# Performance work log

Hardware: AMD Instinct MI355X
Metric: run time of the kernel (lower is better)

## Reference

```python
import jax, jax.numpy as jnp
import numpy as np
import math

N_HEAD = 16
ROPE_BASE = 10000.0

def _rope_cos_sin(seq_len, head_dim, dtype):
    inv_freq = 1.0 / (ROPE_BASE ** (jnp.arange(0, head_dim, 2, dtype=jnp.float32) / head_dim))
    t = jnp.arange(seq_len, dtype=jnp.float32)
    freqs = t[:, None] * inv_freq[None, :]            # [S, D/2]
    emb = jnp.concatenate([freqs, freqs], axis=-1)     # [S, D]
    # broadcast shape [1, 1, S, D] to match q/k [B, H, S, D]
    return jnp.cos(emb)[None, None].astype(dtype), jnp.sin(emb)[None, None].astype(dtype)

def _rotate_half(x):
    x1, x2 = jnp.split(x, 2, axis=-1)
    return jnp.concatenate([-x2, x1], axis=-1)

def setup_inputs() -> dict:
    key = jax.random.key(0)
    ks = jax.random.split(key, 5)
    B, S, E = 2, 2048, 1024
    x = jax.random.normal(ks[0], (B, S, E), dtype=jnp.float32)
    init = 1.0 / math.sqrt(E)
    Wq = jax.random.normal(ks[1], (E, E), dtype=jnp.float32) * init
    Wk = jax.random.normal(ks[2], (E, E), dtype=jnp.float32) * init
    Wv = jax.random.normal(ks[3], (E, E), dtype=jnp.float32) * init
    Wo = jax.random.normal(ks[4], (E, E), dtype=jnp.float32) * init
    # causal mask: True = masked (masked_fill with -inf)
    attn_mask = jnp.triu(jnp.ones((S, S), dtype=bool), k=1)
    return {"x": x, "Wq": Wq, "Wk": Wk, "Wv": Wv, "Wo": Wo, "attn_mask": attn_mask}

def reference(x, Wq, Wk, Wv, Wo, attn_mask):
    B, S, E = x.shape
    H = N_HEAD
    D = E // H
    # projections (torch Linear: y = x @ W.T), split heads -> [B, H, S, D]
    def proj(W):
        return jnp.einsum('bse,fe->bsf', x, W).reshape(B, S, H, D).transpose(0, 2, 1, 3)
    q, k, v = proj(Wq), proj(Wk), proj(Wv)
    cos, sin = _rope_cos_sin(S, D, x.dtype)
    q = q * cos + _rotate_half(q) * sin
    k = k * cos + _rotate_half(k) * sin
    scale = 1.0 / math.sqrt(D)
    scores = jnp.einsum('bhqd,bhkd->bhqk', q, k) * scale  # [B, H, S, S]
    scores = jnp.where(attn_mask[None, None], -jnp.inf, scores)
    attn = jax.nn.softmax(scores, axis=-1)
    out = jnp.einsum('bhqk,bhkd->bhqd', attn, v)           # [B, H, S, D]
    out = out.transpose(0, 2, 1, 3).reshape(B, S, E)
    return jnp.einsum('bse,fe->bsf', out, Wo)
```

## Files before the change

### kernel.cpp

```cpp
#include <hip/hip_runtime.h>
#include <hip/hip_bf16.h>

#define NB 2
#define NH 16
#define SEQ 2048
#define HD 64
#define EMB 1024

typedef unsigned short u16;
typedef unsigned int u32;
typedef __attribute__((ext_vector_type(8))) short bf16x8;
typedef __attribute__((ext_vector_type(4))) float f32x4;
typedef __attribute__((ext_vector_type(8))) unsigned short us8;
typedef __attribute__((ext_vector_type(4))) unsigned short us4;

__device__ __forceinline__ float b2f(u16 u) {
    union { unsigned int i; float f; } v; v.i = ((unsigned int)u) << 16; return v.f;
}
__device__ __forceinline__ u16 f2b(float f) {
    union { float f; unsigned int i; } v; v.f = f;
    unsigned int x = v.i;
    return (u16)((x + 0x7FFFu + ((x >> 16) & 1u)) >> 16);
}
__device__ __forceinline__ u32 pk2(float a, float b) {
    union { __hip_bfloat162 h; u32 u; } v;
    v.h = __float22bfloat162_rn(make_float2(a, b));
    return v.u;
}

__device__ __forceinline__ void gld16(const u16* g, u16* l) {
    __builtin_amdgcn_global_load_lds((const __attribute__((address_space(1))) void*)g,
                                     (__attribute__((address_space(3))) void*)l, 16, 0, 0);
}

#define BAR8P()  asm volatile("s_barrier" ::: "memory")
#define VMW8P(n) asm volatile("s_waitcnt vmcnt(" #n ")" ::: "memory")

__device__ __forceinline__ void conv8(const void* src, u16* dst, int i, int isbf16) {
    if (isbf16) {
        *reinterpret_cast<uint4*>(dst + i) =
            *reinterpret_cast<const uint4*>((const u16*)src + i);
    } else {
        const float* s = (const float*)src + i;
        float4 a = *reinterpret_cast<const float4*>(s);
        float4 b = *reinterpret_cast<const float4*>(s + 4);
        us8 v;
        v[0] = f2b(a.x); v[1] = f2b(a.y); v[2] = f2b(a.z); v[3] = f2b(a.w);
        v[4] = f2b(b.x); v[5] = f2b(b.y); v[6] = f2b(b.z); v[7] = f2b(b.w);
        *reinterpret_cast<us8*>(dst + i) = v;
    }
}

__global__ __launch_bounds__(256)
void prep_54571854463007(const void* __restrict__ x,
                         const void* __restrict__ w0, const void* __restrict__ w1,
                         const void* __restrict__ w2, const void* __restrict__ w3,
                         u16* __restrict__ xb, u16* __restrict__ dqkv,
                         u16* __restrict__ dob, int* __restrict__ flag) {
    __shared__ int cnt;
    if (threadIdx.x == 0) cnt = 0;
    __syncthreads();
    const u16 v = ((const u16*)x)[threadIdx.x];
    const int e = (v >> 7) & 0xFF;
    if (e >= 110 && e <= 135) atomicAdd(&cnt, 1);
    __syncthreads();
    const int isbf16 = (cnt >= 200) ? 1 : 0;
    const int blk = blockIdx.x;
    if (blk == 0 && threadIdx.x == 0) *flag = isbf16;
    const int NXB = (NB * SEQ * EMB) / 2048;
    if (blk < NXB) {
        conv8(x, xb, (blk * 256 + threadIdx.x) * 8, isbf16);
    } else {
        const int r = blk - NXB;
        const int seg = r >> 9;
        const int NW = EMB * EMB;
        const void* src = (seg == 0) ? w0 : (seg == 1) ? w1 : (seg == 2) ? w2 : w3;
        u16* dst = (seg < 3) ? (dqkv + (size_t)seg * NW) : dob;
        conv8(src, dst, ((r & 511) * 256 + threadIdx.x) * 8, isbf16);
    }
}

template<int MIH, int NIH>
__device__ __forceinline__ void quad8p(const bf16x8 (&aT)[4][2], const bf16x8 (&bT)[4][2],
                                       f32x4 (&acc)[8][4]) {
#pragma unroll
    for (int i = 0; i < 4; ++i)
#pragma unroll
        for (int j = 0; j < 2; ++j)
#pragma unroll
            for (int k = 0; k < 2; ++k)
                acc[MIH * 4 + i][NIH * 2 + j] = __builtin_amdgcn_mfma_f32_16x16x32_bf16(
                    aT[i][k], bT[NIH * 2 + j][k], acc[MIH * 4 + i][NIH * 2 + j], 0, 0, 0);
}

__device__ __forceinline__ void rd8p(const u16* Ls, int buf, int rbase, int quad, int fr,
                                     bf16x8 (&dst)[4][2]) {
#pragma unroll
    for (int i = 0; i < 4; ++i) {
        const int R  = rbase + i * 16 + fr;
        const int rb = buf * 16384 + R * 64;
        const int sw = R & 7;
        dst[i][0] = *reinterpret_cast<const bf16x8*>(&Ls[rb + ((quad    ) ^ sw) * 8]);
        dst[i][1] = *reinterpret_cast<const bf16x8*>(&Ls[rb + ((quad + 4) ^ sw) * 8]);
    }
}

__global__ __launch_bounds__(512, 2)
void gemm8p_54571854463007(const u16* __restrict__ A, const u16* __restrict__ Bw,
                           u16* __restrict__ C) {
    __shared__ __align__(16) u16 As[32768];
    __shared__ __align__(16) u16 Bs[32768];
    const int tid  = threadIdx.x;
    const int w    = tid >> 6, lane = tid & 63;
    const int quad = lane >> 4, fr = lane & 15;
    const int wm   = w >> 2, wn = w & 3;
    const int m0   = blockIdx.y * 256, n0 = blockIdx.x * 256;
    const int srow = tid >> 3;
    const int schk = ((tid & 7) ^ (srow & 7)) * 8;

    auto stageU = [&](const u16* G, u16* Ls, int T, int jp, int gbase) {
        const int Tm  = T & 15;
        const int buf = T & 1;
        const int j0  = jp * 2;
        gld16(G + (size_t)(gbase + j0 * 64      + srow) * 1024 + Tm * 64 + schk,
              &Ls[buf * 16384 +  j0      * 4096 + w * 512]);
        gld16(G + (size_t)(gbase + j0 * 64 + 64 + srow) * 1024 + Tm * 64 + schk,
              &Ls[buf * 16384 + (j0 + 1) * 4096 + w * 512]);
    };

    f32x4 acc[8][4];
    const f32x4 zz = {0.f, 0.f, 0.f, 0.f};
#pragma unroll
    for (int i = 0; i < 8; ++i)
#pragma unroll
        for (int j = 0; j < 4; ++j) acc[i][j] = zz;

    stageU(A, As, 0, 0, m0);
    stageU(A, As, 0, 1, m0);
    stageU(Bw, Bs, 0, 0, n0);
    stageU(Bw, Bs, 0, 1, n0);
    stageU(A, As, 1, 0, m0);
    VMW8P(2);
    BAR8P();

#pragma unroll 1
    for (int it = 0; it < 8; ++it) {
        const int ta = 2 * it, tb = ta + 1;
        bf16x8 aT[4][2], bT[4][2];
        rd8p(As, 0, wm * 128, quad, fr, aT);
        rd8p(Bs, 0, wn * 64, quad, fr, bT);
        stageU(A, As, tb, 1, m0);
        __builtin_amdgcn_s_setprio(1); quad8p<0, 0>(aT, bT, acc); __builtin_amdgcn_s_setprio(0);
        BAR8P();
        stageU(Bw, Bs, tb, 0, n0);
        __builtin_amdgcn_s_setprio(1); quad8p<0, 1>(aT, bT, acc); __builtin_amdgcn_s_setprio(0);
        BAR8P();
        rd8p(As, 0, wm * 128 + 64, quad, fr, aT);
        stageU(Bw, Bs, tb, 1, n0);
        __builtin_amdgcn_s_setprio(1); quad8p<1, 0>(aT, bT, acc); __builtin_amdgcn_s_setprio(0);
        BAR8P();
        stageU(A, As, ta + 2, 0, m0);
        __builtin_amdgcn_s_setprio(1); quad8p<1, 1>(aT, bT, acc); __builtin_amdgcn_s_setprio(0);
        VMW8P(2);
        BAR8P();
        rd8p(As, 1, wm * 128, quad, fr, aT);
        rd8p(Bs, 1, wn * 64, quad, fr, bT);
        stageU(A, As, ta + 2, 1, m0);
        __builtin_amdgcn_s_setprio(1); quad8p<0, 0>(aT, bT, acc); __builtin_amdgcn_s_setprio(0);
        BAR8P();
        stageU(Bw, Bs, ta + 2, 0, n0);
        __builtin_amdgcn_s_setprio(1); quad8p<0, 1>(aT, bT, acc); __builtin_amdgcn_s_setprio(0);
        BAR8P();
        rd8p(As, 1, wm * 128 + 64, quad, fr, aT);
        stageU(Bw, Bs, ta + 2, 1, n0);
        __builtin_amdgcn_s_setprio(1); quad8p<1, 0>(aT, bT, acc); __builtin_amdgcn_s_setprio(0);
        BAR8P();
        stageU(A, As, tb + 2, 0, m0);
        __builtin_amdgcn_s_setprio(1); quad8p<1, 1>(aT, bT, acc); __builtin_amdgcn_s_setprio(0);
        VMW8P(2);
        BAR8P();
    }

    const int t0 = n0 >> 10;
    if (t0 == 0) {
        const float SCL = 0.18033688011112042f;
#pragma unroll
        for (int mi = 0; mi < 8; ++mi)
#pragma unroll
            for (int ni = 0; ni < 4; ++ni)
#pragma unroll
                for (int r = 0; r < 4; ++r) acc[mi][ni][r] *= SCL;
    }
    if (t0 < 2) {
        const float inv0 = __powf(10000.f, -(float)fr / 32.f);
        const float inv1 = __powf(10000.f, -(float)(fr + 16) / 32.f);
#pragma unroll
        for (int mi = 0; mi < 8; ++mi)
#pragma unroll
            for (int r = 0; r < 4; ++r) {
                const int s = (m0 + wm * 128 + mi * 16 + quad * 4 + r) & (SEQ - 1);
#pragma unroll
                for (int nl = 0; nl < 2; ++nl) {
                    float sn, cs;
                    __sincosf((float)s * (nl ? inv1 : inv0), &sn, &cs);
                    const float lo = acc[mi][nl][r], hi = acc[mi][nl + 2][r];
                    acc[mi][nl][r]     = lo * cs - hi * sn;
                    acc[mi][nl + 2][r] = hi * cs + lo * sn;
                }
            }
    }
    const size_t TS = (size_t)NB * NH * SEQ * HD;
#pragma unroll
    for (int mi = 0; mi < 8; ++mi)
#pragma unroll
        for (int ni = 0; ni < 4; ++ni)
#pragma unroll
            for (int r = 0; r < 4; ++r) {
                const int m = m0 + wm * 128 + mi * 16 + quad * 4 + r;
                const int n = n0 + wn * 64 + ni * 16 + fr;
                const int t = n >> 10, idx = n & 1023;
                const int h = idx >> 6, d = idx & 63;
                const int b = m >> 11, s = m & (SEQ - 1);
                C[t * TS + ((((size_t)b * NH + h) * SEQ + s) << 6) + d] = f2b(acc[mi][ni][r]);
            }
}

template<int OUT_MODE>
__global__ __launch_bounds__(256)
void gemm_mfma_54571854463007(const u16* __restrict__ A, const u16* __restrict__ Bw,
                              void* __restrict__ C, const int* __restrict__ flagp,
                              int M, int N, int K) {
    __shared__ __align__(16) u16 As[128 * 32];
    __shared__ __align__(16) u16 Bs[128 * 32];
    const int tid  = threadIdx.x;
    const int wave = tid >> 6, lane = tid & 63;
    const int quad = lane >> 4, fr = lane & 15;
    const int wr = (wave >> 1) * 64, wc = (wave & 1) * 64;
    const int m0 = blockIdx.y * 128, n0 = blockIdx.x * 128;
    const int r0 = tid >> 2;
    const int kc = (tid & 3) * 8;
    const f32x4 zz = {0.f, 0.f, 0.f, 0.f};
    f32x4 acc[4][4];
#pragma unroll
    for (int i = 0; i < 4; ++i)
#pragma unroll
        for (int j = 0; j < 4; ++j) acc[i][j] = zz;

    for (int k0 = 0; k0 < K; k0 += 32) {
        gld16(A  + (size_t)(m0 + r0) * K + k0 + kc,      &As[wave * 512]);
        gld16(A  + (size_t)(m0 + 64 + r0) * K + k0 + kc, &As[2048 + wave * 512]);
        gld16(Bw + (size_t)(n0 + r0) * K + k0 + kc,      &Bs[wave * 512]);
        gld16(Bw + (size_t)(n0 + 64 + r0) * K + k0 + kc, &Bs[2048 + wave * 512]);
        __syncthreads();
        bf16x8 af[4], bfr[4];
#pragma unroll
        for (int mi = 0; mi < 4; ++mi)
            af[mi] = *reinterpret_cast<const bf16x8*>(&As[(wr + mi * 16 + fr) * 32 + quad * 8]);
#pragma unroll
        for (int ni = 0; ni < 4; ++ni)
            bfr[ni] = *reinterpret_cast<const bf16x8*>(&Bs[(wc + ni * 16 + fr) * 32 + quad * 8]);
#pragma unroll
        for (int mi = 0; mi < 4; ++mi)
#pragma unroll
            for (int ni = 0; ni < 4; ++ni)
                acc[mi][ni] = __builtin_amdgcn_mfma_f32_16x16x32_bf16(af[mi], bfr[ni], acc[mi][ni], 0, 0, 0);
        __syncthreads();
    }

    const int isbf16 = *flagp;
#pragma unroll
    for (int mi = 0; mi < 4; ++mi)
#pragma unroll
        for (int ni = 0; ni < 4; ++ni)
#pragma unroll
            for (int r = 0; r < 4; ++r) {
                const int m = m0 + wr + mi * 16 + quad * 4 + r;
                const int n = n0 + wc + ni * 16 + fr;
                const float v = acc[mi][ni][r];
                if (isbf16) ((u16*)C)[(size_t)m * N + n] = f2b(v);
                else        ((float*)C)[(size_t)m * N + n] = v;
            }
}

__global__ __launch_bounds__(512, 6)
void flash_54571854463007(const u16* __restrict__ Q, const u16* __restrict__ K,
                          const u16* __restrict__ V, u16* __restrict__ AO,
                          float* __restrict__ OP0, float* __restrict__ OP1,
                          float* __restrict__ LP0, float* __restrict__ LP1) {
    __shared__ __align__(16) u16 Kt[2 * 4096];
    __shared__ __align__(16) u16 Vt[2 * 4608];
    const int tid  = threadIdx.x;
    const int w    = tid >> 6, lane = tid & 63;
    const int quad = lane >> 4, fr = lane & 15;
    const int lin = blockIdx.x;
    const int xcd = lin & 7;
    const int r_  = lin >> 3;
    const int b4  = r_ & 3;
    const int ti  = r_ >> 2;
    int T, kt0, kt1;
    if (ti < 8)       { T = 8 + ti; kt0 = 0;  kt1 = 15; }
    else if (ti == 8) { T = 15;     kt0 = 16; kt1 = 31; }
    else if (ti == 9) { T = 7;      kt0 = 0;  kt1 = 15; }
    else {
        const int g = ti - 10, s = 7 - (g >> 1);
        if ((g & 1) == 0) { T = s + 7; kt0 = 16; kt1 = 2 * T + 1; }
        else              { T = s - 1; kt0 = 0;  kt1 = 2 * T + 1; }
    }
    const bool split = (T >= 8);
    const int bh = xcd * 4 + b4;
    const int h = bh & 15, b = bh >> 4;
    const size_t base = ((size_t)b * NH + h) * SEQ * HD;
    const int k2   = (tid & 31) * 2;
    const int key0 = (k2 & 3) * 16 + (k2 >> 2);
    const int d4   = ((tid >> 5) & 15) * 4;

    const int krs = lane >> 3;
    const int kch = ((lane & 7) ^ krs) * 8;
    const int swz = fr & 7;
    const int co0 = (quad ^ swz) * 8;
    const int co1 = ((quad + 4) ^ swz) * 8;

    const bf16x8 ones = {(short)0x3F80, (short)0x3F80, (short)0x3F80, (short)0x3F80,
                         (short)0x3F80, (short)0x3F80, (short)0x3F80, (short)0x3F80};

    const u16* qp = Q + base + (size_t)(T * 128 + w * 16 + fr) * HD + quad * 8;
    const bf16x8 aq0 = *reinterpret_cast<const bf16x8*>(qp);
    const bf16x8 aq1 = *reinterpret_cast<const bf16x8*>(qp + 32);

    gld16(K + base + (size_t)(kt0 * 64 + w * 8 + krs) * HD + kch, &Kt[w * 512]);
    us4 vc0, vc1, vn0, vn1;
    {
        const u16* vs = V + base + (size_t)(kt0 * 64 + key0) * HD + d4;
        vc0 = *reinterpret_cast<const us4*>(vs);
        vc1 = *reinterpret_cast<const us4*>(vs + 16 * HD);
    }

    const f32x4 zz = {0.f, 0.f, 0.f, 0.f};
    f32x4 lacc = zz;
    f32x4 oacc[4];
#pragma unroll
    for (int nt = 0; nt < 4; ++nt) oacc[nt] = zz;

    for (int kt = kt0; kt <= kt1; ++kt) {
        const int buf = (kt - kt0) & 1;
        const int vb  = buf * 4608;
        const int kb  = buf * 4096;
#pragma unroll
        for (int jj = 0; jj < 4; ++jj) {
            const u32 pk = ((u32)(u16)vc1[jj] << 16) | (u32)(u16)vc0[jj];
            *reinterpret_cast<u32*>(&Vt[vb + (d4 + jj) * 72 + k2]) = pk;
        }
        __syncthreads();
        if (kt + 1 <= kt1) {
            const int kb1 = (buf ^ 1) * 4096;
            gld16(K + base + (size_t)((kt + 1) * 64 + w * 8 + krs) * HD + kch,
                  &Kt[kb1 + w * 512]);
            const u16* vs = V + base + (size_t)((kt + 1) * 64 + key0) * HD + d4;
            vn0 = *reinterpret_cast<const us4*>(vs);
            vn1 = *reinterpret_cast<const us4*>(vs + 16 * HD);
        }
        f32x4 sa[4];
        __builtin_amdgcn_s_setprio(1);
#pragma unroll
        for (int nt = 0; nt < 4; ++nt) {
            const int rb = kb + (nt * 16 + fr) * 64;
            const bf16x8 ka0 = *reinterpret_cast<const bf16x8*>(&Kt[rb + co0]);
            const bf16x8 ka1 = *reinterpret_cast<const bf16x8*>(&Kt[rb + co1]);
            sa[nt] = __builtin_amdgcn_mfma_f32_16x16x32_bf16(ka0, aq0, zz, 0, 0, 0);
            sa[nt] = __builtin_amdgcn_mfma_f32_16x16x32_bf16(ka1, aq1, sa[nt], 0, 0, 0);
        }
        __builtin_amdgcn_s_setprio(0);
        const int dk = kt - 2 * T;
        if (dk >= 0) {
#pragma unroll
            for (int nt = 0; nt < 4; ++nt)
#pragma unroll
                for (int r = 0; r < 4; ++r)
                    if (dk * 64 + nt * 16 + quad * 4 + r > w * 16 + fr)
                        sa[nt][r] = -__builtin_inff();
        }
        u32 c01[4], c23[4];
#pragma unroll
        for (int r = 0; r < 4; ++r) {
            c01[r] = pk2(exp2f(sa[0][r]), exp2f(sa[1][r]));
            c23[r] = pk2(exp2f(sa[2][r]), exp2f(sa[3][r]));
        }
        union { u32 u[4]; bf16x8 v; } P0, P1;
        {
            auto a = __builtin_amdgcn_permlane16_swap(c01[0], c01[2], false, false);
            auto bsw = __builtin_amdgcn_permlane32_swap(a[0], a[1], false, false);
            P0.u[0] = (u32)bsw[0]; P1.u[0] = (u32)bsw[1];
        }
        {
            auto a = __builtin_amdgcn_permlane16_swap(c23[0], c23[2], false, false);
            auto bsw = __builtin_amdgcn_permlane32_swap(a[0], a[1], false, false);
            P0.u[1] = (u32)bsw[0]; P1.u[1] = (u32)bsw[1];
        }
        {
            auto a = __builtin_amdgcn_permlane16_swap(c01[1], c01[3], false, false);
            auto bsw = __builtin_amdgcn_permlane32_swap(a[0], a[1], false, false);
            P0.u[2] = (u32)bsw[0]; P1.u[2] = (u32)bsw[1];
        }
        {
            auto a = __builtin_amdgcn_permlane16_swap(c23[1], c23[3], false, false);
            auto bsw = __builtin_amdgcn_permlane32_swap(a[0], a[1], false, false);
            P0.u[3] = (u32)bsw[0]; P1.u[3] = (u32)bsw[1];
        }
        const bf16x8 pa0 = P0.v;
        const bf16x8 pa1 = P1.v;
        __builtin_amdgcn_s_setprio(1);
        lacc = __builtin_amdgcn_mfma_f32_16x16x32_bf16(pa0, ones, lacc, 0, 0, 0);
        lacc = __builtin_amdgcn_mfma_f32_16x16x32_bf16(pa1, ones, lacc, 0, 0, 0);
#pragma unroll
        for (int nt = 0; nt < 4; ++nt) {
            const bf16x8 bv0 = *reinterpret_cast<const bf16x8*>(&Vt[vb + (nt * 16 + fr) * 72 + quad * 8]);
            const bf16x8 bv1 = *reinterpret_cast<const bf16x8*>(&Vt[vb + (nt * 16 + fr) * 72 + 32 + quad * 8]);
            oacc[nt] = __builtin_amdgcn_mfma_f32_16x16x32_bf16(pa0, bv0, oacc[nt], 0, 0, 0);
            oacc[nt] = __builtin_amdgcn_mfma_f32_16x16x32_bf16(pa1, bv1, oacc[nt], 0, 0, 0);
        }
        __builtin_amdgcn_s_setprio(0);
        vc0 = vn0; vc1 = vn1;
    }
    if (!split) {
#pragma unroll
        for (int r = 0; r < 4; ++r) {
            const float inv = 1.0f / lacc[r];
            const int q = T * 128 + w * 16 + quad * 4 + r;
#pragma unroll
            for (int nt = 0; nt < 4; ++nt)
                AO[(((size_t)b * SEQ + q) * NH + h) * HD + nt * 16 + fr] = f2b(oacc[nt][r] * inv);
        }
    } else {
        float* OP = (kt0 == 16) ? OP1 : OP0;
        float* LP = (kt0 == 16) ? LP1 : LP0;
#pragma unroll
        for (int r = 0; r < 4; ++r) {
            const int row0 = bh * 1024 + (T * 128 + w * 16 + quad * 4 + r) - 1024;
            LP[row0] = lacc[r];
#pragma unroll
            for (int nt = 0; nt < 4; ++nt)
                OP[(size_t)row0 * 64 + nt * 16 + fr] = oacc[nt][r];
        }
    }
}

__global__ __launch_bounds__(256)
void combine_54571854463007(const float* __restrict__ OP0, const float* __restrict__ OP1,
                            const float* __restrict__ LP0, const float* __restrict__ LP1,
                            u16* __restrict__ AO) {
    const int idx  = blockIdx.x * 256 + threadIdx.x;
    const int row  = idx >> 3;
    const int d8   = (idx & 7) * 8;
    const int bh   = row >> 10;
    const int qoff = row & 1023;
    const int h = bh & 15, b = bh >> 4;
    const int q = 1024 + qoff;
    const float4* A = reinterpret_cast<const float4*>(&OP0[(size_t)row * 64 + d8]);
    const float4* Bp = reinterpret_cast<const float4*>(&OP1[(size_t)row * 64 + d8]);
    const float4 a0 = A[0], a1 = A[1], b0 = Bp[0], b1 = Bp[1];
    const float inv = 1.0f / (LP0[row] + LP1[row]);
    us8 o;
    o[0] = f2b((a0.x + b0.x) * inv); o[1] = f2b((a0.y + b0.y) * inv);
    o[2] = f2b((a0.z + b0.z) * inv); o[3] = f2b((a0.w + b0.w) * inv);
    o[4] = f2b((a1.x + b1.x) * inv); o[5] = f2b((a1.y + b1.y) * inv);
    o[6] = f2b((a1.z + b1.z) * inv); o[7] = f2b((a1.w + b1.w) * inv);
    *reinterpret_cast<us8*>(&AO[(((size_t)b * SEQ + q) * NH + h) * HD + d8]) = o;
}

extern "C" void kernel_launch(void* const* d_in, const int* in_sizes, int n_in,
                              void* d_out, int out_size, void* d_ws, size_t ws_size,
                              hipStream_t stream) {
    (void)in_sizes; (void)n_in; (void)out_size; (void)ws_size;
    const void* x  = d_in[0];
    const void* Wq = d_in[1];
    const void* Wk = d_in[2];
    const void* Wv = d_in[3];
    const void* Wo = d_in[4];

    char* ws = (char*)d_ws;
    const size_t MB = 1024 * 1024;
    int* flag = (int*)ws;
    u16* xb   = (u16*)(ws + 64);
    u16* Wqkv = (u16*)(ws + 64 + 8 * MB);
    u16* Wob  = (u16*)(ws + 64 + 14 * MB);
    u16* Qb   = (u16*)(ws + 64 + 16 * MB);
    u16* Kb   = (u16*)(ws + 64 + 24 * MB);
    u16* Vb   = (u16*)(ws + 64 + 32 * MB);
    float* OP0 = (float*)(ws + 64 + 40 * MB);
    float* OP1 = (float*)(ws + 64 + 48 * MB);
    float* LP0 = (float*)(ws + 64 + 56 * MB);
    float* LP1 = (float*)(ws + 64 + 56 * MB + 256 * 1024);
    u16* AO   = xb;

    prep_54571854463007<<<dim3(4096), 256, 0, stream>>>(
        x, Wq, Wk, Wv, Wo, xb, Wqkv, Wob, flag);

    const int M = NB * SEQ;
    gemm8p_54571854463007<<<dim3(3 * EMB / 256, M / 256), 512, 0, stream>>>(
        xb, Wqkv, Qb);

    flash_54571854463007<<<dim3(768), 512, 0, stream>>>(Qb, Kb, Vb, AO,
                                                        OP0, OP1, LP0, LP1);
    combine_54571854463007<<<dim3(1024), 256, 0, stream>>>(OP0, OP1, LP0, LP1, AO);

    gemm_mfma_54571854463007<0><<<dim3(EMB / 128, M / 128), 256, 0, stream>>>(
        AO, Wob, d_out, flag, M, EMB, EMB);
}
```

Baseline: 206.9 us.

## Software-pipeline attention loop: overlap next tile's QK^T/softmax with current PV

Restructures the flash-attention inner loop so the QK^T scores and exp/permlane packing for key tile kt+1 are computed while the PV MFMAs for tile kt are issued. A prologue computes the first tile's P and a separate epilogue handles the last tile. K and V are now prefetched two tiles ahead into double buffers. The aim is to hide the exp/permute latency behind MFMA work, at the cost of more live registers (two sets of P fragments) and a more delicate buffer-reuse and sync ordering.

```diff
diff --git a/kernel.cpp b/kernel.cpp
--- a/kernel.cpp
+++ b/kernel.cpp
@@ -327,39 +327,11 @@
     const bf16x8 aq0 = *reinterpret_cast<const bf16x8*>(qp);
     const bf16x8 aq1 = *reinterpret_cast<const bf16x8*>(qp + 32);
 
-    gld16(K + base + (size_t)(kt0 * 64 + w * 8 + krs) * HD + kch, &Kt[w * 512]);
-    us4 vc0, vc1, vn0, vn1;
-    {
-        const u16* vs = V + base + (size_t)(kt0 * 64 + key0) * HD + d4;
-        vc0 = *reinterpret_cast<const us4*>(vs);
-        vc1 = *reinterpret_cast<const us4*>(vs + 16 * HD);
-    }
-
     const f32x4 zz = {0.f, 0.f, 0.f, 0.f};
-    f32x4 lacc = zz;
-    f32x4 oacc[4];
-#pragma unroll
-    for (int nt = 0; nt < 4; ++nt) oacc[nt] = zz;
-
-    for (int kt = kt0; kt <= kt1; ++kt) {
-        const int buf = (kt - kt0) & 1;
-        const int vb  = buf * 4608;
-        const int kb  = buf * 4096;
-#pragma unroll
-        for (int jj = 0; jj < 4; ++jj) {
-            const u32 pk = ((u32)(u16)vc1[jj] << 16) | (u32)(u16)vc0[jj];
-            *reinterpret_cast<u32*>(&Vt[vb + (d4 + jj) * 72 + k2]) = pk;
-        }
-        __syncthreads();
-        if (kt + 1 <= kt1) {
-            const int kb1 = (buf ^ 1) * 4096;
-            gld16(K + base + (size_t)((kt + 1) * 64 + w * 8 + krs) * HD + kch,
-                  &Kt[kb1 + w * 512]);
-            const u16* vs = V + base + (size_t)((kt + 1) * 64 + key0) * HD + d4;
-            vn0 = *reinterpret_cast<const us4*>(vs);
-            vn1 = *reinterpret_cast<const us4*>(vs + 16 * HD);
-        }
+
+    auto qkt_sm = [&](int kbuf, int ktArg, bf16x8& opa0, bf16x8& opa1) {
         f32x4 sa[4];
+        const int kb = kbuf * 4096;
         __builtin_amdgcn_s_setprio(1);
 #pragma unroll
         for (int nt = 0; nt < 4; ++nt) {
@@ -370,7 +342,7 @@
             sa[nt] = __builtin_amdgcn_mfma_f32_16x16x32_bf16(ka1, aq1, sa[nt], 0, 0, 0);
         }
         __builtin_amdgcn_s_setprio(0);
-        const int dk = kt - 2 * T;
+        const int dk = ktArg - 2 * T;
         if (dk >= 0) {
 #pragma unroll
             for (int nt = 0; nt < 4; ++nt)
@@ -406,8 +378,78 @@
             auto bsw = __builtin_amdgcn_permlane32_swap(a[0], a[1], false, false);
             P0.u[3] = (u32)bsw[0]; P1.u[3] = (u32)bsw[1];
         }
-        const bf16x8 pa0 = P0.v;
-        const bf16x8 pa1 = P1.v;
+        opa0 = P0.v; opa1 = P1.v;
+    };
+
+    us4 vc0, vc1, vn0, vn1;
+    f32x4 lacc = zz;
+    f32x4 oacc[4];
+#pragma unroll
+    for (int nt = 0; nt < 4; ++nt) oacc[nt] = zz;
+
+    gld16(K + base + (size_t)(kt0 * 64 + w * 8 + krs) * HD + kch, &Kt[w * 512]);
+    {
+        const u16* vs = V + base + (size_t)(kt0 * 64 + key0) * HD + d4;
+        vc0 = *reinterpret_cast<const us4*>(vs);
+        vc1 = *reinterpret_cast<const us4*>(vs + 16 * HD);
+    }
+    __syncthreads();
+#pragma unroll
+    for (int jj = 0; jj < 4; ++jj) {
+        const u32 pk = ((u32)(u16)vc1[jj] << 16) | (u32)(u16)vc0[jj];
+        *reinterpret_cast<u32*>(&Vt[(d4 + jj) * 72 + k2]) = pk;
+    }
+    gld16(K + base + (size_t)((kt0 + 1) * 64 + w * 8 + krs) * HD + kch, &Kt[4096 + w * 512]);
+    {
+        const u16* vs = V + base + (size_t)((kt0 + 1) * 64 + key0) * HD + d4;
+        vn0 = *reinterpret_cast<const us4*>(vs);
+        vn1 = *reinterpret_cast<const us4*>(vs + 16 * HD);
+    }
+    bf16x8 pa0, pa1;
+    qkt_sm(0, kt0, pa0, pa1);
+    vc0 = vn0; vc1 = vn1;
+
+    for (int kt = kt0; kt < kt1; ++kt) {
+        const int par = (kt - kt0) & 1;
+        __syncthreads();
+        if (kt + 2 <= kt1) {
+            gld16(K + base + (size_t)((kt + 2) * 64 + w * 8 + krs) * HD + kch,
+                  &Kt[par * 4096 + w * 512]);
+            const u16* vs = V + base + (size_t)((kt + 2) * 64 + key0) * HD + d4;
+            vn0 = *reinterpret_cast<const us4*>(vs);
+            vn1 = *reinterpret_cast<const us4*>(vs + 16 * HD);
+        }
+        {
+            const int vb1 = (par ^ 1) * 4608;
+#pragma unroll
+            for (int jj = 0; jj < 4; ++jj) {
+                const u32 pk = ((u32)(u16)vc1[jj] << 16) | (u32)(u16)vc0[jj];
+                *reinterpret_cast<u32*>(&Vt[vb1 + (d4 + jj) * 72 + k2]) = pk;
+            }
+        }
+        bf16x8 npa0, npa1;
+        qkt_sm(par ^ 1, kt + 1, npa0, npa1);
+        {
+            const int vb = par * 4608;
+            __builtin_amdgcn_s_setprio(1);
+            lacc = __builtin_amdgcn_mfma_f32_16x16x32_bf16(pa0, ones, lacc, 0, 0, 0);
+            lacc = __builtin_amdgcn_mfma_f32_16x16x32_bf16(pa1, ones, lacc, 0, 0, 0);
+#pragma unroll
+            for (int nt = 0; nt < 4; ++nt) {
+                const bf16x8 bv0 = *reinterpret_cast<const bf16x8*>(&Vt[vb + (nt * 16 + fr) * 72 + quad * 8]);
+                const bf16x8 bv1 = *reinterpret_cast<const bf16x8*>(&Vt[vb + (nt * 16 + fr) * 72 + 32 + quad * 8]);
+                oacc[nt] = __builtin_amdgcn_mfma_f32_16x16x32_bf16(pa0, bv0, oacc[nt], 0, 0, 0);
+                oacc[nt] = __builtin_amdgcn_mfma_f32_16x16x32_bf16(pa1, bv1, oacc[nt], 0, 0, 0);
+            }
+            __builtin_amdgcn_s_setprio(0);
+        }
+        pa0 = npa0; pa1 = npa1;
+        vc0 = vn0; vc1 = vn1;
+    }
+    {
+        const int par = (kt1 - kt0) & 1;
+        __syncthreads();
+        const int vb = par * 4608;
         __builtin_amdgcn_s_setprio(1);
         lacc = __builtin_amdgcn_mfma_f32_16x16x32_bf16(pa0, ones, lacc, 0, 0, 0);
         lacc = __builtin_amdgcn_mfma_f32_16x16x32_bf16(pa1, ones, lacc, 0, 0, 0);
@@ -419,7 +461,6 @@
             oacc[nt] = __builtin_amdgcn_mfma_f32_16x16x32_bf16(pa1, bv1, oacc[nt], 0, 0, 0);
         }
         __builtin_amdgcn_s_setprio(0);
-        vc0 = vn0; vc1 = vn1;
     }
     if (!split) {
 #pragma unroll
```

Result: no change. 210.5 us (+1.7%).
